# Kernel optimization log

Hardware: AMD Instinct MI355X
Metric: run time of the kernel (lower is better)

The kernel has to match this reference:

```python
import jax, jax.numpy as jnp
import numpy as np

BETA = 0.9      # LIF leak factor
THR = 1.0       # firing threshold
SLOPE = 5.0     # surrogate-gradient sigmoid slope


def spike_fn(v):
    # Heaviside forward, sigmoid surrogate gradient (straight-through).
    hard = (v > THR).astype(v.dtype)
    surr = jax.nn.sigmoid(SLOPE * (v - THR))
    return hard + (surr - jax.lax.stop_gradient(surr))


def setup_inputs() -> dict:
    key = jax.random.key(0)
    ks = jax.random.split(key, 4)
    B, T, IN, H, OUT = 16, 128, 1024, 4096, 1024
    def lin_w(k, out_d, in_d):
        bound = 1.0 / np.sqrt(in_d)
        return jax.random.uniform(k, (out_d, in_d), jnp.float32, -bound, bound)
    return {
        "x": jax.random.normal(ks[0], (B, T, IN), jnp.float32),
        "w1": lin_w(ks[1], H, IN), "b1": jnp.zeros((H,), jnp.float32),
        "w2": lin_w(ks[2], H, H),  "b2": jnp.zeros((H,), jnp.float32),
        "w3": lin_w(ks[3], OUT, H), "b3": jnp.zeros((OUT,), jnp.float32),
    }


def reference(x, w1, b1, w2, b2, w3, b3):
    # x: [B, T, IN]; sequential per-timestep SNN feed-forward, readout = sum over time.
    B = x.shape[0]
    H = w1.shape[0]
    v0 = jnp.zeros((B, H), x.dtype)

    def step(carry, xt):                      # xt: [B, IN]
        v1, v2 = carry
        h1 = xt @ w1.T + b1                   # [B, H]
        v1 = BETA * v1 + h1
        s1 = spike_fn(v1)
        v1 = v1 - s1 * THR                    # soft reset
        h2 = s1 @ w2.T + b2                   # [B, H]
        v2 = BETA * v2 + h2
        s2 = spike_fn(v2)
        v2 = v2 - s2 * THR
        logits = s2 @ w3.T + b3               # [B, OUT]
        return (v1, v2), logits

    _, logits = jax.lax.scan(step, (v0, v0), jnp.swapaxes(x, 0, 1))  # [T, B, OUT]
    return logits.sum(axis=0)                 # readout_mode == 'sum'
```

## Files before the change

### kernel.cpp

```cpp
#include <hip/hip_runtime.h>
#include <hip/hip_bf16.h>

#define B_   16
#define T_   128
#define IN_  1024
#define H_   4096
#define OUT_ 1024
#define M_   (B_ * T_)

typedef __attribute__((ext_vector_type(8))) short short8;
typedef __attribute__((ext_vector_type(4))) float f32x4;
typedef __attribute__((ext_vector_type(4))) int i32x4;
typedef __attribute__((ext_vector_type(4))) unsigned short u16x4;
typedef unsigned short u16;
typedef signed char i8;

__device__ inline u16 f2bf_rne(float f) {
  unsigned u = __float_as_uint(f);
  unsigned r = u + 0x7FFFu + ((u >> 16) & 1u);
  return (u16)(r >> 16);
}
__device__ inline float bf2f(u16 s) {
  return __uint_as_float(((unsigned)s) << 16);
}
__device__ inline int pack4(int a, int b, int c, int d) {
  return (a & 255) | ((b & 255) << 8) | ((c & 255) << 16) | ((d & 255) << 24);
}

__device__ inline void xcd_swizzle(int bid0, int& bnI, int& bmI) {
  const int xcd = bid0 & 7;
  const int loc = bid0 >> 3;
  bnI = (xcd & 3) * 8 + (loc & 7);
  bmI = (xcd >> 2) * 8 + (loc >> 3);
}

#define NX_  (M_ * IN_)
#define NW1_ (H_ * IN_)
#define NW2_ (H_ * H_)

__device__ inline void split4bf(const float4 f, u16* __restrict__ hi,
                                u16* __restrict__ lo, size_t e) {
  u16x4 h, l;
  h.x = f2bf_rne(f.x); l.x = f2bf_rne(f.x - bf2f(h.x));
  h.y = f2bf_rne(f.y); l.y = f2bf_rne(f.y - bf2f(h.y));
  h.z = f2bf_rne(f.z); l.z = f2bf_rne(f.z - bf2f(h.z));
  h.w = f2bf_rne(f.w); l.w = f2bf_rne(f.w - bf2f(h.w));
  *(u16x4*)(hi + e) = h;
  *(u16x4*)(lo + e) = l;
}

__device__ inline void splitw2_1(float w, int& c0, int& c1, int& c2) {
  int wf = __float2int_rn(w * 268435456.0f);
  c0 = (wf + 32768) >> 16;
  int r0 = wf - (c0 << 16);
  if (r0 >= 32640) { c0 += 1; r0 -= 65536; }
  c1 = (r0 + 128) >> 8;
  c2 = r0 - (c1 << 8);
}

__global__ void split_xw1_kernel(const float4* __restrict__ x,
                                 const float4* __restrict__ w1,
                                 u16* __restrict__ xh, u16* __restrict__ xl,
                                 u16* __restrict__ w1h, u16* __restrict__ w1l) {
  const int total4 = (NX_ + NW1_) / 4;
  for (int i = blockIdx.x * blockDim.x + threadIdx.x; i < total4;
       i += gridDim.x * blockDim.x) {
    if (i < NX_ / 4) {
      split4bf(x[i], xh, xl, (size_t)i * 4);
    } else {
      int j = i - NX_ / 4;
      split4bf(w1[j], w1h, w1l, (size_t)j * 4);
    }
  }
}

#define BK1 64

__global__ __launch_bounds__(256, 2) void gemm1_rec(
    const u16* __restrict__ Ah, const u16* __restrict__ Al,
    const u16* __restrict__ Bh, const u16* __restrict__ Bl,
    const float* __restrict__ bias, i8* __restrict__ s1out,
    const float4* __restrict__ w2src,
    i8* __restrict__ p0, i8* __restrict__ p1, i8* __restrict__ p2) {
  __shared__ __align__(16) char smem[65536];
  u16* sAh = (u16*)smem;
  u16* sAl = (u16*)(smem + 16384);
  u16* sBh = (u16*)(smem + 32768);
  u16* sBl = (u16*)(smem + 49152);

  const int tid  = threadIdx.x;
  const int lane = tid & 63;
  const int wid  = tid >> 6;
  const int wm   = (wid >> 1) * 64;
  const int wn   = (wid & 1) * 64;
  const int bid  = blockIdx.y * 32 + blockIdx.x;
  int bnI, bmI;
  xcd_swizzle(bid, bnI, bmI);
  const int bm = bmI * 128;
  const int bn = bnI * 128;

  const int sdst = (tid & 7) * 8;
  const int scol = (((tid & 7) ^ ((tid >> 3) & 7)) * 8);
  const int q8   = (lane >> 4) * 8;
  const int rsw  = (lane & 7) * 8;

  f32x4 acc[4][4];
#pragma unroll
  for (int i = 0; i < 4; ++i)
#pragma unroll
    for (int j = 0; j < 4; ++j) acc[i][j] = (f32x4){0.f, 0.f, 0.f, 0.f};

  const int wbase = bid * 8192 + tid * 2;
  float4 wfa = w2src[wbase];
  float4 wfb = w2src[wbase + 1];

#pragma unroll 1
  for (int it = 0; it < IN_ / BK1; ++it) {
    const int kt = it * BK1;
    __syncthreads();
#pragma unroll
    for (int l = 0; l < 4; ++l) {
      int row = l * 32 + (tid >> 3);
      size_t ga = (size_t)(bm + row) * IN_ + kt + scol;
      size_t gb = (size_t)(bn + row) * IN_ + kt + scol;
      int ld = row * BK1 + sdst;
      __builtin_amdgcn_global_load_lds(
          (const __attribute__((address_space(1))) unsigned int*)(Ah + ga),
          (__attribute__((address_space(3))) unsigned int*)(&sAh[ld]), 16, 0, 0);
      __builtin_amdgcn_global_load_lds(
          (const __attribute__((address_space(1))) unsigned int*)(Al + ga),
          (__attribute__((address_space(3))) unsigned int*)(&sAl[ld]), 16, 0, 0);
      __builtin_amdgcn_global_load_lds(
          (const __attribute__((address_space(1))) unsigned int*)(Bh + gb),
          (__attribute__((address_space(3))) unsigned int*)(&sBh[ld]), 16, 0, 0);
      __builtin_amdgcn_global_load_lds(
          (const __attribute__((address_space(1))) unsigned int*)(Bl + gb),
          (__attribute__((address_space(3))) unsigned int*)(&sBl[ld]), 16, 0, 0);
    }
    __syncthreads();

    const int nit = (it + 1 < 16) ? it + 1 : 15;
    float4 nfa = w2src[wbase + nit * 512];
    float4 nfb = w2src[wbase + nit * 512 + 1];

    {
      const int sbase = bid * 8192 + it * 512 + tid * 2;
#pragma unroll
      for (int u = 0; u < 2; ++u) {
        float4 f = u ? wfb : wfa;
        int a0, a1, a2, b0, b1, b2, c0, c1, c2, d0, d1, d2;
        splitw2_1(f.x, a0, a1, a2);
        splitw2_1(f.y, b0, b1, b2);
        splitw2_1(f.z, c0, c1, c2);
        splitw2_1(f.w, d0, d1, d2);
        size_t e = (size_t)(sbase + u) * 4;
        *(int*)(p0 + e) = pack4(a0, b0, c0, d0);
        *(int*)(p1 + e) = pack4(a1, b1, c1, d1);
        *(int*)(p2 + e) = pack4(a2, b2, c2, d2);
      }
    }

#pragma unroll
    for (int ks = 0; ks < BK1; ks += 32) {
      const int swz = (ks + q8) ^ rsw;
      short8 ah[4], al[4], bh[4], bl[4];
#pragma unroll
      for (int i = 0; i < 4; ++i) {
        int ro = (wm + i * 16 + (lane & 15)) * BK1 + swz;
        ah[i] = *(const short8*)&sAh[ro];
        al[i] = *(const short8*)&sAl[ro];
      }
#pragma unroll
      for (int j = 0; j < 4; ++j) {
        int ro = (wn + j * 16 + (lane & 15)) * BK1 + swz;
        bh[j] = *(const short8*)&sBh[ro];
        bl[j] = *(const short8*)&sBl[ro];
      }
#pragma unroll
      for (int i = 0; i < 4; ++i)
#pragma unroll
        for (int j = 0; j < 4; ++j) {
          acc[i][j] = __builtin_amdgcn_mfma_f32_16x16x32_bf16(ah[i], bh[j], acc[i][j], 0, 0, 0);
          acc[i][j] = __builtin_amdgcn_mfma_f32_16x16x32_bf16(ah[i], bl[j], acc[i][j], 0, 0, 0);
          acc[i][j] = __builtin_amdgcn_mfma_f32_16x16x32_bf16(al[i], bh[j], acc[i][j], 0, 0, 0);
          acc[i][j] = __builtin_amdgcn_mfma_f32_16x16x32_bf16(al[i], bl[j], acc[i][j], 0, 0, 0);
        }
    }

    wfa = nfa;
    wfb = nfb;
  }

  float* hl = (float*)smem;
  const int c = tid & 127;
  const float bv = bias[bn + c];
  float v = 0.0f;
  __syncthreads();
#pragma unroll
  for (int half = 0; half < 2; ++half) {
    if (wm == half * 64) {
#pragma unroll
      for (int i = 0; i < 4; ++i)
#pragma unroll
        for (int j = 0; j < 4; ++j) {
          int col = wn + j * 16 + (lane & 15);
#pragma unroll
          for (int r = 0; r < 4; ++r) {
            int lrow = i * 16 + (lane >> 4) * 4 + r;
            hl[lrow * 128 + col] = acc[i][j][r];
          }
        }
    }
    __syncthreads();
    if (tid < 128) {
      for (int tt = 0; tt < 64; ++tt) {
        float h = hl[tt * 128 + c] + bv;
        v = 0.9f * v + h;
        i8 sp = 0;
        if (v > 1.0f) { sp = 1; v -= 1.0f; }
        s1out[(size_t)(bm + half * 64 + tt) * H_ + bn + c] = sp;
      }
    }
    __syncthreads();
  }
}

#define G2_GLD(srcp, ldsp)                                                  \
  __builtin_amdgcn_global_load_lds(                                         \
      (const __attribute__((address_space(1))) unsigned int*)(srcp),        \
      (__attribute__((address_space(3))) unsigned int*)(ldsp), 16, 0, 0)

__global__ __launch_bounds__(256, 2) void gemm2_i8(
    const i8* __restrict__ A,
    const i8* __restrict__ P0, const i8* __restrict__ P1,
    const i8* __restrict__ P2,
    const float* __restrict__ bias, float* __restrict__ s2out) {
  __shared__ __align__(16) char smem[40960];
  i8* sA  = (i8*)smem;
  i8* sB1 = (i8*)(smem + 16384);
  i8* sB2 = (i8*)(smem + 24576);
  i8* sB0 = (i8*)(smem + 32768);

  const int tid  = threadIdx.x;
  const int lane = tid & 63;
  const int wid  = tid >> 6;
  const int wm   = (wid >> 1) * 64;
  const int wn   = (wid & 1) * 32;

  const int bid = blockIdx.x;
  const int xcd = bid & 7, loc = bid >> 3;
  const int bnI = xcd * 8 + (loc & 7);
  const int bmI = loc >> 3;
  const int bm = bmI * 128, bn = bnI * 64;

  const int q16  = (lane >> 4) * 16;
  const int r15  = lane & 15;
  const int rswb = (lane & 7) * 16;

  const int sdstB = (tid & 7) * 16;
  const int scolB = (((tid & 7) ^ ((tid >> 3) & 7)) * 16);
  const int strow = tid >> 3;

  i32x4 acc0[4][2], acc1[4][2], acc2[4][2];
#pragma unroll
  for (int i = 0; i < 4; ++i)
#pragma unroll
    for (int j = 0; j < 2; ++j) {
      acc0[i][j] = (i32x4){0, 0, 0, 0};
      acc1[i][j] = (i32x4){0, 0, 0, 0};
      acc2[i][j] = (i32x4){0, 0, 0, 0};
    }

#pragma unroll 1
  for (int kt = 0; kt < H_; kt += 128) {
    __syncthreads();
#pragma unroll
    for (int l = 0; l < 4; ++l) {
      int row = l * 32 + strow;
      G2_GLD(A + (size_t)(bm + row) * H_ + kt + scolB, sA + row * 128 + sdstB);
    }
#pragma unroll
    for (int l = 0; l < 2; ++l) {
      int row = l * 32 + strow;
      int ld  = row * 128 + sdstB;
      size_t g = (size_t)(bn + row) * H_ + kt + scolB;
      G2_GLD(P1 + g, sB1 + ld);
      G2_GLD(P2 + g, sB2 + ld);
      G2_GLD(P0 + g, sB0 + ld);
    }
    __syncthreads();

#pragma unroll
    for (int ks = 0; ks < 2; ++ks) {
      const int swz = (ks * 64 + q16) ^ rswb;
      i32x4 a[4], b1[2], b2[2], b0[2];
#pragma unroll
      for (int i = 0; i < 4; ++i)
        a[i] = *(const i32x4*)(sA + (wm + i * 16 + r15) * 128 + swz);
#pragma unroll
      for (int j = 0; j < 2; ++j) {
        int ro = (wn + j * 16 + r15) * 128 + swz;
        b1[j] = *(const i32x4*)(sB1 + ro);
        b2[j] = *(const i32x4*)(sB2 + ro);
        b0[j] = *(const i32x4*)(sB0 + ro);
      }
#pragma unroll
      for (int i = 0; i < 4; ++i)
#pragma unroll
        for (int j = 0; j < 2; ++j) {
          acc1[i][j] = __builtin_amdgcn_mfma_i32_16x16x64_i8(a[i], b1[j], acc1[i][j], 0, 0, 0);
          acc2[i][j] = __builtin_amdgcn_mfma_i32_16x16x64_i8(a[i], b2[j], acc2[i][j], 0, 0, 0);
          acc0[i][j] = __builtin_amdgcn_mfma_i32_16x16x64_i8(a[i], b0[j], acc0[i][j], 0, 0, 0);
        }
    }
  }

  f32x4 facc[4][2];
#pragma unroll
  for (int i = 0; i < 4; ++i)
#pragma unroll
    for (int j = 0; j < 2; ++j)
#pragma unroll
      for (int r = 0; r < 4; ++r)
        facc[i][j][r] = 0x1p-28f * (float)((acc1[i][j][r] << 8) + acc2[i][j][r]) +
                        0x1p-12f * (float)acc0[i][j][r];

  float* hl = (float*)smem;
  const int c = tid & 63;
  const float bv = bias[bn + c];
  float v = 0.0f, cnt = 0.0f;
  __syncthreads();
#pragma unroll
  for (int half = 0; half < 2; ++half) {
    if (wm == half * 64) {
#pragma unroll
      for (int i = 0; i < 4; ++i)
#pragma unroll
        for (int j = 0; j < 2; ++j) {
          int col = wn + j * 16 + (lane & 15);
#pragma unroll
          for (int r = 0; r < 4; ++r) {
            int lrow = i * 16 + (lane >> 4) * 4 + r;
            hl[lrow * 64 + col] = facc[i][j][r];
          }
        }
    }
    __syncthreads();
    if (tid < 64) {
      for (int tt = 0; tt < 64; ++tt) {
        float h = hl[tt * 64 + c] + bv;
        v = 0.9f * v + h;
        if (v > 1.0f) { cnt += 1.0f; v -= 1.0f; }
      }
    }
    __syncthreads();
  }
  if (tid < 64) s2out[(size_t)bmI * H_ + bn + c] = cnt;
}

__global__ void out_gemm_kernel(const float* __restrict__ s2sum,
                                const float* __restrict__ w3,
                                const float* __restrict__ b3,
                                float* __restrict__ out) {
  int o = blockIdx.x;
  int lane = threadIdx.x;
  float acc[B_];
#pragma unroll
  for (int b = 0; b < B_; ++b) acc[b] = 0.f;
  const float* wrow = w3 + (size_t)o * H_;
  for (int i = 0; i < H_ / 64; ++i) {
    float w = wrow[i * 64 + lane];
#pragma unroll
    for (int b = 0; b < B_; ++b)
      acc[b] += w * s2sum[b * H_ + i * 64 + lane];
  }
#pragma unroll
  for (int b = 0; b < B_; ++b) {
    float v = acc[b];
#pragma unroll
    for (int off = 32; off > 0; off >>= 1) v += __shfl_xor(v, off);
    if (lane == b) out[b * OUT_ + o] = v + (float)T_ * b3[o];
  }
}

extern "C" void kernel_launch(void* const* d_in, const int* in_sizes, int n_in,
                              void* d_out, int out_size, void* d_ws, size_t ws_size,
                              hipStream_t stream) {
  const float* x  = (const float*)d_in[0];
  const float* w1 = (const float*)d_in[1];
  const float* b1 = (const float*)d_in[2];
  const float* w2 = (const float*)d_in[3];
  const float* b2 = (const float*)d_in[4];
  const float* w3 = (const float*)d_in[5];
  const float* b3 = (const float*)d_in[6];
  float* out = (float*)d_out;

  char* ws = (char*)d_ws;
  i8*    s1    = (i8*)(ws);
  u16*   x_hi  = (u16*)(ws + 8388608);
  u16*   x_lo  = (u16*)(ws + 12582912);
  u16*   w1_hi = (u16*)(ws + 16777216);
  u16*   w1_lo = (u16*)(ws + 25165824);
  i8*    w2p0  = (i8*)(ws + 33554432);
  i8*    w2p1  = (i8*)(ws + 50331648);
  i8*    w2p2  = (i8*)(ws + 67108864);
  float* s2sum = (float*)(ws + 83886080);

  split_xw1_kernel<<<1024, 256, 0, stream>>>((const float4*)x, (const float4*)w1,
                                             x_hi, x_lo, w1_hi, w1_lo);

  dim3 g1(H_ / 128, M_ / 128);
  gemm1_rec<<<g1, 256, 0, stream>>>(x_hi, x_lo, w1_hi, w1_lo, b1, s1,
                                    (const float4*)w2, w2p0, w2p1, w2p2);

  gemm2_i8<<<dim3(1024), 256, 0, stream>>>(s1, w2p0, w2p1, w2p2, b2, s2sum);

  out_gemm_kernel<<<OUT_, 64, 0, stream>>>(s2sum, w3, b3, out);
}
```

Baseline: 184.3 us.

## Halve gemm2 tile width to 128x32 and raise occupancy to four blocks

The int8 GEMM2 tile shrinks from 128x64 to 128x32, each wave now covering 32 rows by all 32 columns. Grid size doubles to 2048 blocks, LDS drops to 28 KB, and launch bounds request 4 blocks per CU. B fragments are loaded one plane at a time so fewer registers are live. The aim is more latency hiding and better CU fill, but the A tile is reloaded twice as often, raising global and LDS traffic per MFMA. The block-to-tile mapping is also reordered so each XCD handles whole row slabs.

```diff
diff --git a/kernel.cpp b/kernel.cpp
--- a/kernel.cpp
+++ b/kernel.cpp
@@ -230,28 +230,27 @@
       (const __attribute__((address_space(1))) unsigned int*)(srcp),        \
       (__attribute__((address_space(3))) unsigned int*)(ldsp), 16, 0, 0)
 
-__global__ __launch_bounds__(256, 2) void gemm2_i8(
+__global__ __launch_bounds__(256, 4) void gemm2_i8(
     const i8* __restrict__ A,
     const i8* __restrict__ P0, const i8* __restrict__ P1,
     const i8* __restrict__ P2,
     const float* __restrict__ bias, float* __restrict__ s2out) {
-  __shared__ __align__(16) char smem[40960];
+  __shared__ __align__(16) char smem[28672];
   i8* sA  = (i8*)smem;
   i8* sB1 = (i8*)(smem + 16384);
-  i8* sB2 = (i8*)(smem + 24576);
-  i8* sB0 = (i8*)(smem + 32768);
+  i8* sB2 = (i8*)(smem + 20480);
+  i8* sB0 = (i8*)(smem + 24576);
 
   const int tid  = threadIdx.x;
   const int lane = tid & 63;
   const int wid  = tid >> 6;
-  const int wm   = (wid >> 1) * 64;
-  const int wn   = (wid & 1) * 32;
+  const int wm   = wid * 32;
 
   const int bid = blockIdx.x;
   const int xcd = bid & 7, loc = bid >> 3;
-  const int bnI = xcd * 8 + (loc & 7);
-  const int bmI = loc >> 3;
-  const int bm = bmI * 128, bn = bnI * 64;
+  const int bmI = xcd * 2 + (loc >> 7);
+  const int bnI = loc & 127;
+  const int bm = bmI * 128, bn = bnI * 32;
 
   const int q16  = (lane >> 4) * 16;
   const int r15  = lane & 15;
@@ -261,9 +260,9 @@
   const int scolB = (((tid & 7) ^ ((tid >> 3) & 7)) * 16);
   const int strow = tid >> 3;
 
-  i32x4 acc0[4][2], acc1[4][2], acc2[4][2];
-#pragma unroll
-  for (int i = 0; i < 4; ++i)
+  i32x4 acc0[2][2], acc1[2][2], acc2[2][2];
+#pragma unroll
+  for (int i = 0; i < 2; ++i)
 #pragma unroll
     for (int j = 0; j < 2; ++j) {
       acc0[i][j] = (i32x4){0, 0, 0, 0};
@@ -279,11 +278,9 @@
       int row = l * 32 + strow;
       G2_GLD(A + (size_t)(bm + row) * H_ + kt + scolB, sA + row * 128 + sdstB);
     }
-#pragma unroll
-    for (int l = 0; l < 2; ++l) {
-      int row = l * 32 + strow;
-      int ld  = row * 128 + sdstB;
-      size_t g = (size_t)(bn + row) * H_ + kt + scolB;
+    {
+      size_t g = (size_t)(bn + strow) * H_ + kt + scolB;
+      int ld = strow * 128 + sdstB;
       G2_GLD(P1 + g, sB1 + ld);
       G2_GLD(P2 + g, sB2 + ld);
       G2_GLD(P0 + g, sB0 + ld);
@@ -293,31 +290,40 @@
 #pragma unroll
     for (int ks = 0; ks < 2; ++ks) {
       const int swz = (ks * 64 + q16) ^ rswb;
-      i32x4 a[4], b1[2], b2[2], b0[2];
-#pragma unroll
-      for (int i = 0; i < 4; ++i)
+      i32x4 a[2], b[2];
+#pragma unroll
+      for (int i = 0; i < 2; ++i)
         a[i] = *(const i32x4*)(sA + (wm + i * 16 + r15) * 128 + swz);
 #pragma unroll
-      for (int j = 0; j < 2; ++j) {
-        int ro = (wn + j * 16 + r15) * 128 + swz;
-        b1[j] = *(const i32x4*)(sB1 + ro);
-        b2[j] = *(const i32x4*)(sB2 + ro);
-        b0[j] = *(const i32x4*)(sB0 + ro);
-      }
-#pragma unroll
-      for (int i = 0; i < 4; ++i)
-#pragma unroll
-        for (int j = 0; j < 2; ++j) {
-          acc1[i][j] = __builtin_amdgcn_mfma_i32_16x16x64_i8(a[i], b1[j], acc1[i][j], 0, 0, 0);
-          acc2[i][j] = __builtin_amdgcn_mfma_i32_16x16x64_i8(a[i], b2[j], acc2[i][j], 0, 0, 0);
-          acc0[i][j] = __builtin_amdgcn_mfma_i32_16x16x64_i8(a[i], b0[j], acc0[i][j], 0, 0, 0);
-        }
-    }
-  }
-
-  f32x4 facc[4][2];
-#pragma unroll
-  for (int i = 0; i < 4; ++i)
+      for (int j = 0; j < 2; ++j)
+        b[j] = *(const i32x4*)(sB1 + (j * 16 + r15) * 128 + swz);
+#pragma unroll
+      for (int i = 0; i < 2; ++i)
+#pragma unroll
+        for (int j = 0; j < 2; ++j)
+          acc1[i][j] = __builtin_amdgcn_mfma_i32_16x16x64_i8(a[i], b[j], acc1[i][j], 0, 0, 0);
+#pragma unroll
+      for (int j = 0; j < 2; ++j)
+        b[j] = *(const i32x4*)(sB2 + (j * 16 + r15) * 128 + swz);
+#pragma unroll
+      for (int i = 0; i < 2; ++i)
+#pragma unroll
+        for (int j = 0; j < 2; ++j)
+          acc2[i][j] = __builtin_amdgcn_mfma_i32_16x16x64_i8(a[i], b[j], acc2[i][j], 0, 0, 0);
+#pragma unroll
+      for (int j = 0; j < 2; ++j)
+        b[j] = *(const i32x4*)(sB0 + (j * 16 + r15) * 128 + swz);
+#pragma unroll
+      for (int i = 0; i < 2; ++i)
+#pragma unroll
+        for (int j = 0; j < 2; ++j)
+          acc0[i][j] = __builtin_amdgcn_mfma_i32_16x16x64_i8(a[i], b[j], acc0[i][j], 0, 0, 0);
+    }
+  }
+
+  f32x4 facc[2][2];
+#pragma unroll
+  for (int i = 0; i < 2; ++i)
 #pragma unroll
     for (int j = 0; j < 2; ++j)
 #pragma unroll
@@ -326,36 +332,36 @@
                         0x1p-12f * (float)acc0[i][j][r];
 
   float* hl = (float*)smem;
-  const int c = tid & 63;
+  const int c = tid & 31;
   const float bv = bias[bn + c];
   float v = 0.0f, cnt = 0.0f;
   __syncthreads();
 #pragma unroll
   for (int half = 0; half < 2; ++half) {
-    if (wm == half * 64) {
-#pragma unroll
-      for (int i = 0; i < 4; ++i)
+    if ((wm & 64) == half * 64) {
+#pragma unroll
+      for (int i = 0; i < 2; ++i)
 #pragma unroll
         for (int j = 0; j < 2; ++j) {
-          int col = wn + j * 16 + (lane & 15);
+          int col = j * 16 + r15;
 #pragma unroll
           for (int r = 0; r < 4; ++r) {
-            int lrow = i * 16 + (lane >> 4) * 4 + r;
-            hl[lrow * 64 + col] = facc[i][j][r];
+            int lrow = (wm & 32) + i * 16 + (lane >> 4) * 4 + r;
+            hl[lrow * 32 + col] = facc[i][j][r];
           }
         }
     }
     __syncthreads();
-    if (tid < 64) {
+    if (tid < 32) {
       for (int tt = 0; tt < 64; ++tt) {
-        float h = hl[tt * 64 + c] + bv;
+        float h = hl[tt * 32 + c] + bv;
         v = 0.9f * v + h;
         if (v > 1.0f) { cnt += 1.0f; v -= 1.0f; }
       }
     }
     __syncthreads();
   }
-  if (tid < 64) s2out[(size_t)bmI * H_ + bn + c] = cnt;
+  if (tid < 32) s2out[(size_t)bmI * H_ + bn + c] = cnt;
 }
 
 __global__ void out_gemm_kernel(const float* __restrict__ s2sum,
@@ -413,7 +419,7 @@
   gemm1_rec<<<g1, 256, 0, stream>>>(x_hi, x_lo, w1_hi, w1_lo, b1, s1,
                                     (const float4*)w2, w2p0, w2p1, w2p2);
 
-  gemm2_i8<<<dim3(1024), 256, 0, stream>>>(s1, w2p0, w2p1, w2p2, b2, s2sum);
+  gemm2_i8<<<dim3(2048), 256, 0, stream>>>(s1, w2p0, w2p1, w2p2, b2, s2sum);
 
   out_gemm_kernel<<<OUT_, 64, 0, stream>>>(s2sum, w3, b3, out);
 }
```

After: 211.7 us. +14.9%, slower.
